# Kernel tuning notes

Measured on AMD Instinct MI355X. Metric: run time of the kernel, lower is better.

The kernel has to match this reference:

```python
import jax, jax.numpy as jnp
import numpy as np

TOKENS, IN_F, OUT_F = 8192, 4096, 4096
MAXQ = 15          # 4-bit
ZERO_POINT = 8     # (maxq + 1) // 2


def _make_24_mask(key, in_f, out_f):
    """Boolean 2:4 mask: exactly 2 True per contiguous group of 4 along in_f."""
    scores = jax.random.normal(key, (in_f // 4, 4, out_f), dtype=jnp.float32)
    # ascending sort along the group-of-4 axis; index 2 = 2nd largest value
    thresh = jnp.sort(scores, axis=1)[:, 2:3, :]
    mask = scores >= thresh  # keeps top-2 of each group of 4
    return mask.reshape(in_f, out_f)


def setup_inputs() -> dict:
    key = jax.random.key(0)
    k_x, k_q, k_m, k_s = jax.random.split(key, 4)
    x = jax.random.normal(k_x, (TOKENS, IN_F), dtype=jnp.float16)
    qvals = jax.random.randint(k_q, (IN_F, OUT_F), 0, MAXQ + 1, dtype=jnp.int32)
    mask = _make_24_mask(k_m, IN_F, OUT_F)
    # per-column scales (groupsize == infeatures -> one scale row)
    scales = (jax.random.uniform(k_s, (1, OUT_F), dtype=jnp.float32) * 0.01 + 0.001).astype(jnp.float16)
    return {"x": x, "qvals": qvals, "mask": mask, "scales": scales}


def reference(x, qvals, mask, scales):
    # Dequantize: W = (q - zero_point) * scale, then apply 2:4 sparsity mask.
    w = (qvals.astype(jnp.float32) - ZERO_POINT) * scales.astype(jnp.float32)  # [in, out]
    w = jnp.where(mask, w, 0.0).astype(x.dtype)
    # GEMM with fp32 accumulation (as the fused kernel does), output in x.dtype
    y = jnp.einsum("ti,io->to", x, w, preferred_element_type=jnp.float32)
    return y.astype(x.dtype)
```

## Files before the change

kernel.cpp:

```cpp
#include <hip/hip_runtime.h>
#include <stdint.h>

typedef short short8 __attribute__((ext_vector_type(8)));
typedef float floatx4 __attribute__((ext_vector_type(4)));

#define M_TOK 8192
#define K_IN  4096
#define N_OUT 4096
#define NTT   (K_IN / 32)

static __device__ __forceinline__ float bf2f(ushort u) {
    union { uint32_t u; float f; } v;
    v.u = ((uint32_t)u) << 16;
    return v.f;
}
static __device__ __forceinline__ ushort f2bf(float f) {
    union { float f; uint32_t u; } v;
    v.f = f;
    uint32_t u = v.u;
    uint32_t r = (u + 0x7FFFu + ((u >> 16) & 1u)) >> 16;
    return (ushort)r;
}

__global__ void detect_zero_kernel(int* __restrict__ flags) {
    if (threadIdx.x < 3) flags[1 + threadIdx.x] = 0;
}

__global__ __launch_bounds__(256) void detect_count_kernel(
    const unsigned char* __restrict__ mb, int* __restrict__ flags) {
    const ushort* mh = (const ushort*)mb;
    const unsigned int* mw = (const unsigned int*)mb;
    __shared__ int sh[3];
    if (threadIdx.x < 3) sh[threadIdx.x] = 0;
    __syncthreads();
    int s = blockIdx.x * 256 + threadIdx.x;
    int grp = s & 255;
    int o   = (s * 97) & 4095;
    int c1 = 0, c2 = 0, c4 = 0;
    #pragma unroll
    for (int r = 0; r < 4; ++r) {
        size_t idx = (size_t)(4 * grp + r) * N_OUT + o;
        c1 += (mb[idx] != 0);
        c2 += (mh[idx] != 0);
        c4 += (mw[idx] != 0);
    }
    if (c1 != 2) atomicAdd(&sh[0], 1);
    if (c2 != 2) atomicAdd(&sh[1], 1);
    if (c4 != 2) atomicAdd(&sh[2], 1);
    __syncthreads();
    if (threadIdx.x == 0) {
        atomicAdd(&flags[1], sh[0]);
        atomicAdd(&flags[2], sh[1]);
        atomicAdd(&flags[3], sh[2]);
    }
}

__global__ void detect_final_kernel(int* __restrict__ flags) {
    if (threadIdx.x == 0) {
        int size = 4, best = flags[3];
        if (flags[2] < best) { size = 2; best = flags[2]; }
        if (flags[1] < best) { size = 1; }
        flags[0] = size;
    }
}

__global__ __launch_bounds__(256) void convert_x_kernel(
    const float* __restrict__ xf, ushort* __restrict__ Xb) {
    const int total = M_TOK * K_IN;
    const int stride = gridDim.x * 256 * 8;
    for (int i = (blockIdx.x * 256 + threadIdx.x) * 8; i < total; i += stride) {
        floatx4 f0 = *(const floatx4*)&xf[i];
        floatx4 f1 = *(const floatx4*)&xf[i + 4];
        short8 v;
        #pragma unroll
        for (int j = 0; j < 4; ++j) v[j]     = (short)f2bf(f0[j]);
        #pragma unroll
        for (int j = 0; j < 4; ++j) v[4 + j] = (short)f2bf(f1[j]);
        *(short8*)&Xb[i] = v;
    }
}

__global__ __launch_bounds__(256) void dequant_kernel(
    const int* __restrict__ q, const void* __restrict__ maskp,
    const float* __restrict__ scales, ushort* __restrict__ Bt,
    const int* __restrict__ flagp) {
    const int msize = flagp[0];
    const int i0 = blockIdx.x * 64;
    const int o0 = blockIdx.y * 64;
    const int tid = threadIdx.x;
    const unsigned char* mb = (const unsigned char*)maskp;
    const ushort* mh = (const ushort*)maskp;
    const unsigned int* mi = (const unsigned int*)maskp;
    __shared__ ushort T[64][72];

    for (int p = 0; p < 16; ++p) {
        int idx = p * 256 + tid;
        int r = idx >> 6, c = idx & 63;
        size_t gi = (size_t)(i0 + r) * N_OUT + (o0 + c);
        bool m;
        if (msize == 1)      m = (mb[gi] != 0);
        else if (msize == 2) m = (mh[gi] != 0);
        else                 m = (mi[gi] != 0);
        float s = scales[o0 + c];
        float w = m ? (float)(q[gi] - 8) * s : 0.0f;
        T[r][c] = f2bf(w);
    }
    __syncthreads();
    for (int p = 0; p < 2; ++p) {
        int ol = p * 32 + (tid >> 3);
        int i8 = (tid & 7) * 8;
        short8 v;
        #pragma unroll
        for (int j = 0; j < 8; ++j) v[j] = (short)T[i8 + j][ol];
        *(short8*)&Bt[(size_t)(o0 + ol) * K_IN + i0 + i8] = v;
    }
}

#define GL2L16(gp, lbase)                                                      \
    __builtin_amdgcn_global_load_lds(                                          \
        (const __attribute__((address_space(1))) void*)(gp),                   \
        (__attribute__((address_space(3))) void*)(lbase), 16, 0, 0)

#define MFMA16(a, b, c) __builtin_amdgcn_mfma_f32_16x16x32_bf16(a, b, c, 0, 0, 0)

__global__ __launch_bounds__(256, 2) void gemm_kernel(
    const ushort* __restrict__ X,
    const ushort* __restrict__ Bt,
    float* __restrict__ Y) {
    __shared__ ushort As[2][128][32];
    __shared__ ushort Bs[2][256][32];

    const int tid  = threadIdx.x;
    const int w    = tid >> 6;
    const int lane = tid & 63;

    const int xcd = blockIdx.x & 7;
    const int jj  = (blockIdx.x >> 3) & 63;
    const int rr0 = blockIdx.x >> 9;
    const int m_tile = rr0 * 32 + (xcd & 1) * 16 + (jj & 15);
    const int n_tile = (xcd >> 1) * 4 + (jj >> 4);
    const int row0 = m_tile * 128;
    const int col0 = n_tile * 256;

    floatx4 acc[8][4] = {};

    const int schunk = (tid & 3) ^ ((tid >> 3) & 3);
    const ushort* gA = X  + (size_t)(row0 + (tid >> 2)) * K_IN + schunk * 8;
    const ushort* gB = Bt + (size_t)(col0 + (tid >> 2)) * K_IN + schunk * 8;

    const int fr = lane & 15, g = lane >> 4;
    const int fsw = (fr >> 1) & 3;

    #define STG(BF, tt)                                                        \
        do {                                                                   \
            GL2L16(gA + (size_t)(tt) * 32,                                     \
                   (char*)&As[BF][w * 16][0] + lane * 16);                     \
            GL2L16(gA + (size_t)64 * K_IN + (size_t)(tt) * 32,                 \
                   (char*)&As[BF][64 + w * 16][0] + lane * 16);                \
            GL2L16(gB + (size_t)(tt) * 32,                                     \
                   (char*)&Bs[BF][w * 16][0] + lane * 16);                     \
            GL2L16(gB + (size_t)64 * K_IN + (size_t)(tt) * 32,                 \
                   (char*)&Bs[BF][64 + w * 16][0] + lane * 16);                \
            GL2L16(gB + (size_t)128 * K_IN + (size_t)(tt) * 32,                \
                   (char*)&Bs[BF][128 + w * 16][0] + lane * 16);               \
            GL2L16(gB + (size_t)192 * K_IN + (size_t)(tt) * 32,                \
                   (char*)&Bs[BF][192 + w * 16][0] + lane * 16);               \
        } while (0)

    #define TILE(BF, T)                                                        \
        do {                                                                   \
            short8 afr[8], bfr[4];                                             \
            _Pragma("unroll")                                                  \
            for (int n = 0; n < 4; ++n)                                        \
                bfr[n] = *(const short8*)&Bs[BF][w * 64 + n * 16 + fr]         \
                             [(g ^ fsw) * 8];                                  \
            _Pragma("unroll")                                                  \
            for (int m = 0; m < 8; ++m)                                        \
                afr[m] = *(const short8*)&As[BF][m * 16 + fr][(g ^ fsw) * 8];  \
            if ((T) + 1 < NTT) STG((BF) ^ 1, (T) + 1);                         \
            __builtin_amdgcn_s_barrier();                                      \
            asm volatile("s_waitcnt lgkmcnt(0)" ::: "memory");                 \
            __builtin_amdgcn_sched_barrier(0);                                 \
            __builtin_amdgcn_s_setprio(1);                                     \
            _Pragma("unroll")                                                  \
            for (int m = 0; m < 8; ++m)                                        \
                _Pragma("unroll")                                              \
                for (int n = 0; n < 4; ++n)                                    \
                    acc[m][n] = MFMA16(afr[m], bfr[n], acc[m][n]);             \
            __builtin_amdgcn_s_setprio(0);                                     \
            asm volatile("s_waitcnt vmcnt(0)" ::: "memory");                   \
            __builtin_amdgcn_s_barrier();                                      \
        } while (0)

    STG(0, 0);
    asm volatile("s_waitcnt vmcnt(0)" ::: "memory");
    __builtin_amdgcn_s_barrier();

    for (int t = 0; t < NTT; t += 2) {
        TILE(0, t);
        TILE(1, t + 1);
    }

    const int fq = lane >> 4;
    #pragma unroll
    for (int m = 0; m < 8; ++m)
        #pragma unroll
        for (int n = 0; n < 4; ++n)
            #pragma unroll
            for (int i = 0; i < 4; ++i) {
                int rr = row0 + m * 16 + fq * 4 + i;
                int cc = col0 + w * 64 + n * 16 + fr;
                Y[(size_t)rr * N_OUT + cc] = acc[m][n][i];
            }
    #undef TILE
    #undef STG
}

__global__ __launch_bounds__(256) void fallback_kernel(
    const float* __restrict__ xf, const int* __restrict__ q,
    const void* __restrict__ maskp, const float* __restrict__ scales,
    float* __restrict__ Y, const int* __restrict__ flagp) {
    const int msize = flagp[0];
    const int o = blockIdx.x * 256 + threadIdx.x;
    const int t = blockIdx.y;
    const unsigned char* mb = (const unsigned char*)maskp;
    const ushort* mh = (const ushort*)maskp;
    const unsigned int* mi = (const unsigned int*)maskp;
    float s = scales[o];
    float acc = 0.f;
    for (int i = 0; i < K_IN; ++i) {
        float x = bf2f(f2bf(xf[(size_t)t * K_IN + i]));
        size_t gi = (size_t)i * N_OUT + o;
        bool m;
        if (msize == 1)      m = (mb[gi] != 0);
        else if (msize == 2) m = (mh[gi] != 0);
        else                 m = (mi[gi] != 0);
        if (m) acc += x * bf2f(f2bf((float)(q[gi] - 8) * s));
    }
    Y[(size_t)t * N_OUT + o] = acc;
}

extern "C" void kernel_launch(void* const* d_in, const int* in_sizes, int n_in,
                              void* d_out, int out_size, void* d_ws, size_t ws_size,
                              hipStream_t stream) {
    const float* x      = (const float*)d_in[0];
    const int*   q      = (const int*)d_in[1];
    const void*  mask   = d_in[2];
    const float* scales = (const float*)d_in[3];
    float* y = (float*)d_out;

    const size_t BT_OFF = 64;
    const size_t XB_OFF = BT_OFF + (size_t)N_OUT * K_IN * 2;
    const size_t need   = XB_OFF + (size_t)M_TOK * K_IN * 2;

    int* flags = (int*)d_ws;
    detect_zero_kernel<<<1, 64, 0, stream>>>(flags);
    detect_count_kernel<<<64, 256, 0, stream>>>(
        (const unsigned char*)mask, flags);
    detect_final_kernel<<<1, 64, 0, stream>>>(flags);

    if (ws_size >= need) {
        ushort* Bt = (ushort*)((char*)d_ws + BT_OFF);
        ushort* Xb = (ushort*)((char*)d_ws + XB_OFF);
        convert_x_kernel<<<4096, 256, 0, stream>>>(x, Xb);
        dequant_kernel<<<dim3(K_IN / 64, N_OUT / 64), 256, 0, stream>>>(
            q, mask, scales, Bt, flags);
        gemm_kernel<<<dim3((M_TOK / 128) * (N_OUT / 256)), 256, 0, stream>>>(
            Xb, Bt, y);
    } else {
        fallback_kernel<<<dim3(N_OUT / 256, M_TOK), 256, 0, stream>>>(
            x, q, mask, scales, y, flags);
    }
}
```

Baseline: 361.6 us.

## Triple-buffer GEMM K-loop and merge prep and detection kernels

The GEMM moves from a double-buffered to a triple-buffered LDS pipeline. Loads are issued two tiles ahead, and each tile ends with a partial vmcnt wait and a single barrier instead of two. The three mask-detection kernels become one single-block kernel that scans only the first group of rows, and x conversion and weight dequantization are merged into one launch. LDS use per block grows, which may hurt occupancy at two blocks per CU, and detection now samples fewer mask groups.

Result: no change. 360.2 us (-0.4%).

```diff
diff --git a/kernel.cpp b/kernel.cpp
--- a/kernel.cpp
+++ b/kernel.cpp
@@ -22,97 +22,84 @@
     return (ushort)r;
 }
 
-__global__ void detect_zero_kernel(int* __restrict__ flags) {
-    if (threadIdx.x < 3) flags[1 + threadIdx.x] = 0;
-}
-
-__global__ __launch_bounds__(256) void detect_count_kernel(
+__global__ __launch_bounds__(256) void detect_kernel(
     const unsigned char* __restrict__ mb, int* __restrict__ flags) {
     const ushort* mh = (const ushort*)mb;
     const unsigned int* mw = (const unsigned int*)mb;
-    __shared__ int sh[3];
-    if (threadIdx.x < 3) sh[threadIdx.x] = 0;
+    __shared__ int v[3];
+    if (threadIdx.x < 3) v[threadIdx.x] = 0;
     __syncthreads();
-    int s = blockIdx.x * 256 + threadIdx.x;
-    int grp = s & 255;
-    int o   = (s * 97) & 4095;
-    int c1 = 0, c2 = 0, c4 = 0;
-    #pragma unroll
-    for (int r = 0; r < 4; ++r) {
-        size_t idx = (size_t)(4 * grp + r) * N_OUT + o;
-        c1 += (mb[idx] != 0);
-        c2 += (mh[idx] != 0);
-        c4 += (mw[idx] != 0);
-    }
-    if (c1 != 2) atomicAdd(&sh[0], 1);
-    if (c2 != 2) atomicAdd(&sh[1], 1);
-    if (c4 != 2) atomicAdd(&sh[2], 1);
+    int l0 = 0, l1 = 0, l2 = 0;
+    for (int o = threadIdx.x; o < 4096; o += 256) {
+        int c1 = 0, c2 = 0, c4 = 0;
+        #pragma unroll
+        for (int r = 0; r < 4; ++r) {
+            int idx = r * N_OUT + o;
+            c1 += (mb[idx] != 0);
+            c2 += (mh[idx] != 0);
+            c4 += (mw[idx] != 0);
+        }
+        l0 += (c1 != 2); l1 += (c2 != 2); l2 += (c4 != 2);
+    }
+    atomicAdd(&v[0], l0); atomicAdd(&v[1], l1); atomicAdd(&v[2], l2);
     __syncthreads();
     if (threadIdx.x == 0) {
-        atomicAdd(&flags[1], sh[0]);
-        atomicAdd(&flags[2], sh[1]);
-        atomicAdd(&flags[3], sh[2]);
-    }
-}
-
-__global__ void detect_final_kernel(int* __restrict__ flags) {
-    if (threadIdx.x == 0) {
-        int size = 4, best = flags[3];
-        if (flags[2] < best) { size = 2; best = flags[2]; }
-        if (flags[1] < best) { size = 1; }
+        int size = 4, best = v[2];
+        if (v[1] < best) { size = 2; best = v[1]; }
+        if (v[0] < best) { size = 1; }
         flags[0] = size;
     }
 }
 
-__global__ __launch_bounds__(256) void convert_x_kernel(
-    const float* __restrict__ xf, ushort* __restrict__ Xb) {
-    const int total = M_TOK * K_IN;
-    const int stride = gridDim.x * 256 * 8;
-    for (int i = (blockIdx.x * 256 + threadIdx.x) * 8; i < total; i += stride) {
-        floatx4 f0 = *(const floatx4*)&xf[i];
-        floatx4 f1 = *(const floatx4*)&xf[i + 4];
-        short8 v;
-        #pragma unroll
-        for (int j = 0; j < 4; ++j) v[j]     = (short)f2bf(f0[j]);
-        #pragma unroll
-        for (int j = 0; j < 4; ++j) v[4 + j] = (short)f2bf(f1[j]);
-        *(short8*)&Xb[i] = v;
-    }
-}
-
-__global__ __launch_bounds__(256) void dequant_kernel(
+__global__ __launch_bounds__(256) void prep_kernel(
+    const float* __restrict__ xf, ushort* __restrict__ Xb,
     const int* __restrict__ q, const void* __restrict__ maskp,
     const float* __restrict__ scales, ushort* __restrict__ Bt,
     const int* __restrict__ flagp) {
-    const int msize = flagp[0];
-    const int i0 = blockIdx.x * 64;
-    const int o0 = blockIdx.y * 64;
     const int tid = threadIdx.x;
-    const unsigned char* mb = (const unsigned char*)maskp;
-    const ushort* mh = (const ushort*)maskp;
-    const unsigned int* mi = (const unsigned int*)maskp;
-    __shared__ ushort T[64][72];
-
-    for (int p = 0; p < 16; ++p) {
-        int idx = p * 256 + tid;
-        int r = idx >> 6, c = idx & 63;
-        size_t gi = (size_t)(i0 + r) * N_OUT + (o0 + c);
-        bool m;
-        if (msize == 1)      m = (mb[gi] != 0);
-        else if (msize == 2) m = (mh[gi] != 0);
-        else                 m = (mi[gi] != 0);
-        float s = scales[o0 + c];
-        float w = m ? (float)(q[gi] - 8) * s : 0.0f;
-        T[r][c] = f2bf(w);
-    }
-    __syncthreads();
-    for (int p = 0; p < 2; ++p) {
-        int ol = p * 32 + (tid >> 3);
-        int i8 = (tid & 7) * 8;
-        short8 v;
-        #pragma unroll
-        for (int j = 0; j < 8; ++j) v[j] = (short)T[i8 + j][ol];
-        *(short8*)&Bt[(size_t)(o0 + ol) * K_IN + i0 + i8] = v;
+    if (blockIdx.x < 4096) {
+        const int total = M_TOK * K_IN;
+        const int stride = 4096 * 256 * 8;
+        for (int i = (blockIdx.x * 256 + tid) * 8; i < total; i += stride) {
+            floatx4 f0 = *(const floatx4*)&xf[i];
+            floatx4 f1 = *(const floatx4*)&xf[i + 4];
+            short8 v;
+            #pragma unroll
+            for (int j = 0; j < 4; ++j) v[j]     = (short)f2bf(f0[j]);
+            #pragma unroll
+            for (int j = 0; j < 4; ++j) v[4 + j] = (short)f2bf(f1[j]);
+            *(short8*)&Xb[i] = v;
+        }
+    } else {
+        const int d  = blockIdx.x - 4096;
+        const int i0 = (d & 63) * 64;
+        const int o0 = (d >> 6) * 64;
+        const int msize = flagp[0];
+        const unsigned char* mb = (const unsigned char*)maskp;
+        const ushort* mh = (const ushort*)maskp;
+        const unsigned int* mi = (const unsigned int*)maskp;
+        __shared__ ushort T[64][72];
+        for (int p = 0; p < 16; ++p) {
+            int idx = p * 256 + tid;
+            int r = idx >> 6, c = idx & 63;
+            size_t gi = (size_t)(i0 + r) * N_OUT + (o0 + c);
+            bool m;
+            if (msize == 1)      m = (mb[gi] != 0);
+            else if (msize == 2) m = (mh[gi] != 0);
+            else                 m = (mi[gi] != 0);
+            float s = scales[o0 + c];
+            float w = m ? (float)(q[gi] - 8) * s : 0.0f;
+            T[r][c] = f2bf(w);
+        }
+        __syncthreads();
+        for (int p = 0; p < 2; ++p) {
+            int ol = p * 32 + (tid >> 3);
+            int i8 = (tid & 7) * 8;
+            short8 v;
+            #pragma unroll
+            for (int j = 0; j < 8; ++j) v[j] = (short)T[i8 + j][ol];
+            *(short8*)&Bt[(size_t)(o0 + ol) * K_IN + i0 + i8] = v;
+        }
     }
 }
 
@@ -127,8 +114,8 @@
     const ushort* __restrict__ X,
     const ushort* __restrict__ Bt,
     float* __restrict__ Y) {
-    __shared__ ushort As[2][128][32];
-    __shared__ ushort Bs[2][256][32];
+    __shared__ ushort As[3][128][32];
+    __shared__ ushort Bs[3][256][32];
 
     const int tid  = threadIdx.x;
     const int w    = tid >> 6;
@@ -151,36 +138,33 @@
     const int fr = lane & 15, g = lane >> 4;
     const int fsw = (fr >> 1) & 3;
 
-    #define STG(BF, tt)                                                        \
+    #define STG(SL, tt)                                                        \
         do {                                                                   \
             GL2L16(gA + (size_t)(tt) * 32,                                     \
-                   (char*)&As[BF][w * 16][0] + lane * 16);                     \
+                   (char*)&As[SL][w * 16][0] + lane * 16);                     \
             GL2L16(gA + (size_t)64 * K_IN + (size_t)(tt) * 32,                 \
-                   (char*)&As[BF][64 + w * 16][0] + lane * 16);                \
+                   (char*)&As[SL][64 + w * 16][0] + lane * 16);                \
             GL2L16(gB + (size_t)(tt) * 32,                                     \
-                   (char*)&Bs[BF][w * 16][0] + lane * 16);                     \
+                   (char*)&Bs[SL][w * 16][0] + lane * 16);                     \
             GL2L16(gB + (size_t)64 * K_IN + (size_t)(tt) * 32,                 \
-                   (char*)&Bs[BF][64 + w * 16][0] + lane * 16);                \
+                   (char*)&Bs[SL][64 + w * 16][0] + lane * 16);                \
             GL2L16(gB + (size_t)128 * K_IN + (size_t)(tt) * 32,                \
-                   (char*)&Bs[BF][128 + w * 16][0] + lane * 16);               \
+                   (char*)&Bs[SL][128 + w * 16][0] + lane * 16);               \
             GL2L16(gB + (size_t)192 * K_IN + (size_t)(tt) * 32,                \
-                   (char*)&Bs[BF][192 + w * 16][0] + lane * 16);               \
+                   (char*)&Bs[SL][192 + w * 16][0] + lane * 16);               \
         } while (0)
 
-    #define TILE(BF, T)                                                        \
+    #define TILE(SL, T, SG, GATE_KIND)                                         \
         do {                                                                   \
             short8 afr[8], bfr[4];                                             \
             _Pragma("unroll")                                                  \
             for (int n = 0; n < 4; ++n)                                        \
-                bfr[n] = *(const short8*)&Bs[BF][w * 64 + n * 16 + fr]         \
+                bfr[n] = *(const short8*)&Bs[SL][w * 64 + n * 16 + fr]         \
                              [(g ^ fsw) * 8];                                  \
             _Pragma("unroll")                                                  \
             for (int m = 0; m < 8; ++m)                                        \
-                afr[m] = *(const short8*)&As[BF][m * 16 + fr][(g ^ fsw) * 8];  \
-            if ((T) + 1 < NTT) STG((BF) ^ 1, (T) + 1);                         \
-            __builtin_amdgcn_s_barrier();                                      \
-            asm volatile("s_waitcnt lgkmcnt(0)" ::: "memory");                 \
-            __builtin_amdgcn_sched_barrier(0);                                 \
+                afr[m] = *(const short8*)&As[SL][m * 16 + fr][(g ^ fsw) * 8];  \
+            if (SG) STG(((SL) + 2) % 3, (T) + 2);                              \
             __builtin_amdgcn_s_setprio(1);                                     \
             _Pragma("unroll")                                                  \
             for (int m = 0; m < 8; ++m)                                        \
@@ -188,18 +172,31 @@
                 for (int n = 0; n < 4; ++n)                                    \
                     acc[m][n] = MFMA16(afr[m], bfr[n], acc[m][n]);             \
             __builtin_amdgcn_s_setprio(0);                                     \
-            asm volatile("s_waitcnt vmcnt(0)" ::: "memory");                   \
-            __builtin_amdgcn_s_barrier();                                      \
+            asm volatile("s_waitcnt lgkmcnt(0)" ::: "memory");                 \
+            if ((GATE_KIND) == 0) {                                            \
+                asm volatile("s_waitcnt vmcnt(6)" ::: "memory");               \
+            } else if ((GATE_KIND) == 1) {                                     \
+                asm volatile("s_waitcnt vmcnt(0)" ::: "memory");               \
+            }                                                                  \
+            if ((GATE_KIND) != 2) {                                            \
+                __builtin_amdgcn_s_barrier();                                  \
+                __builtin_amdgcn_sched_barrier(0);                             \
+            }                                                                  \
         } while (0)
 
     STG(0, 0);
-    asm volatile("s_waitcnt vmcnt(0)" ::: "memory");
+    STG(1, 1);
+    asm volatile("s_waitcnt vmcnt(6)" ::: "memory");
     __builtin_amdgcn_s_barrier();
-
-    for (int t = 0; t < NTT; t += 2) {
-        TILE(0, t);
-        TILE(1, t + 1);
-    }
+    __builtin_amdgcn_sched_barrier(0);
+
+    for (int t = 0; t < 126; t += 3) {
+        TILE(0, t,     true, 0);
+        TILE(1, t + 1, true, 0);
+        TILE(2, t + 2, true, 0);
+    }
+    TILE(0, 126, false, 1);
+    TILE(1, 127, false, 2);
 
     const int fq = lane >> 4;
     #pragma unroll
@@ -254,17 +251,12 @@
     const size_t need   = XB_OFF + (size_t)M_TOK * K_IN * 2;
 
     int* flags = (int*)d_ws;
-    detect_zero_kernel<<<1, 64, 0, stream>>>(flags);
-    detect_count_kernel<<<64, 256, 0, stream>>>(
-        (const unsigned char*)mask, flags);
-    detect_final_kernel<<<1, 64, 0, stream>>>(flags);
+    detect_kernel<<<1, 256, 0, stream>>>((const unsigned char*)mask, flags);
 
     if (ws_size >= need) {
         ushort* Bt = (ushort*)((char*)d_ws + BT_OFF);
         ushort* Xb = (ushort*)((char*)d_ws + XB_OFF);
-        convert_x_kernel<<<4096, 256, 0, stream>>>(x, Xb);
-        dequant_kernel<<<dim3(K_IN / 64, N_OUT / 64), 256, 0, stream>>>(
-            q, mask, scales, Bt, flags);
+        prep_kernel<<<8192, 256, 0, stream>>>(x, Xb, q, mask, scales, Bt, flags);
         gemm_kernel<<<dim3((M_TOK / 128) * (N_OUT / 256)), 256, 0, stream>>>(
             Xb, Bt, y);
     } else {
```
